# Performance work log

Measured on AMD Instinct MI355X. Metric: run time of the kernel, lower is better.

The kernel has to match this reference:

```python
import jax, jax.numpy as jnp
import numpy as np

ALPHA = 0.2  # LeakyReLU negative slope


def setup_inputs() -> dict:
    key = jax.random.key(0)
    k_x, k_w, k_a = jax.random.split(key, 3)
    B, N, F_in = 4, 2048, 128
    H, nhid = 4, 32  # out_channel=128, nheads=4
    x = jax.random.normal(k_x, (B, N, F_in), dtype=jnp.float32)
    # per-head projection and attention vector, xavier-ish scale
    W = jax.random.normal(k_w, (H, F_in, nhid), dtype=jnp.float32) * (1.414 * np.sqrt(2.0 / (F_in + nhid))) / np.sqrt(3.0) * np.sqrt(3.0)
    a = jax.random.normal(k_a, (H, 2 * nhid), dtype=jnp.float32) * (1.414 * np.sqrt(2.0 / (2 * nhid + 1)))
    return {"x": x, "W": W, "a": a}


def reference(x, W, a):
    # x: [B,N,F_in], W: [H,F_in,d], a: [H,2d]
    H = W.shape[0]
    d = W.shape[2]
    B, N, _ = x.shape
    Wh = jnp.einsum('bni,hij->bhnj', x, W)          # [B,H,N,d]
    a1 = a[:, :d]                                    # [H,d]
    a2 = a[:, d:]                                    # [H,d]
    Wh1 = jnp.einsum('bhnd,hd->bhn', Wh, a1)         # [B,H,N]
    Wh2 = jnp.einsum('bhnd,hd->bhn', Wh, a2)         # [B,H,N]
    e = Wh1[:, :, :, None] + Wh2[:, :, None, :]      # [B,H,N,N]
    e = jnp.where(e > 0, e, ALPHA * e)               # LeakyReLU
    attn = jax.nn.softmax(e, axis=-1)                # softmax over source nodes
    h = jnp.einsum('bhij,bhjd->bhid', attn, Wh)      # [B,H,N,d]
    h = jax.nn.elu(h)
    # concat heads along feature dim: [B,N,H*d]
    out = jnp.transpose(h, (0, 2, 1, 3)).reshape(B, N, H * d)
    return out
```

## Files before the change

kernel.cpp:

```cpp
#include <hip/hip_runtime.h>


#define LOG2E 1.4426950408889634f
constexpr int Nn = 2048, Fin = 128, Dd = 32;

typedef _Float16 half8 __attribute__((ext_vector_type(8)));
typedef _Float16 half4v __attribute__((ext_vector_type(4)));
typedef _Float16 half2v __attribute__((ext_vector_type(2)));
typedef float f32x4 __attribute__((ext_vector_type(4)));

union H8 { half2v h2[4]; half8 h8; };

__global__ __launch_bounds__(256) void k1_wh(
    const float* __restrict__ x, const float* __restrict__ W,
    const float* __restrict__ a, _Float16* __restrict__ whT,
    float* __restrict__ sArr, float* __restrict__ tArr) {
  int blk = blockIdx.x;
  int bh = blk >> 5, tile = blk & 31;
  int b = bh >> 2, h = bh & 3;
  int tid = threadIdx.x, w = tid >> 6, lane = tid & 63;
  int q = lane >> 4, m = lane & 15;
  int rowbase = tile * 64 + w * 16;

  const float* Wq = W + h * Fin * Dd;
  const float* xb = x + (size_t)(b * Nn + rowbase + m) * Fin;

  f32x4 acc[2];
  acc[0] = (f32x4){0.f, 0.f, 0.f, 0.f};
  acc[1] = (f32x4){0.f, 0.f, 0.f, 0.f};

#pragma unroll
  for (int kt = 0; kt < 4; ++kt) {
    float4 x0 = *(const float4*)(xb + kt * 32 + q * 8);
    float4 x1 = *(const float4*)(xb + kt * 32 + q * 8 + 4);
    float xv[8] = {x0.x, x0.y, x0.z, x0.w, x1.x, x1.y, x1.z, x1.w};
    half8 Ah, Al;
#pragma unroll
    for (int j = 0; j < 8; ++j) {
      _Float16 hi = (_Float16)xv[j];
      Ah[j] = hi;
      Al[j] = (_Float16)(xv[j] - (float)hi);
    }
#pragma unroll
    for (int nt = 0; nt < 2; ++nt) {
      half8 Bh, Bl;
#pragma unroll
      for (int j = 0; j < 8; ++j) {
        float wv = Wq[(kt * 32 + q * 8 + j) * Dd + nt * 16 + m];
        _Float16 hi = (_Float16)wv;
        Bh[j] = hi;
        Bl[j] = (_Float16)(wv - (float)hi);
      }
      acc[nt] = __builtin_amdgcn_mfma_f32_16x16x32_f16(Ah, Bh, acc[nt], 0, 0, 0);
      acc[nt] = __builtin_amdgcn_mfma_f32_16x16x32_f16(Al, Bh, acc[nt], 0, 0, 0);
      acc[nt] = __builtin_amdgcn_mfma_f32_16x16x32_f16(Ah, Bl, acc[nt], 0, 0, 0);
    }
  }

#pragma unroll
  for (int nt = 0; nt < 2; ++nt) {
    int d = nt * 16 + m;
    half4v h4;
#pragma unroll
    for (int r = 0; r < 4; ++r) h4[r] = (_Float16)acc[nt][r];
    *(half4v*)(whT + (size_t)(bh * Dd + d) * Nn + rowbase + q * 4) = h4;
  }

  const float* ah = a + h * 2 * Dd;
  float a1m0 = ah[m], a1m1 = ah[16 + m];
  float a2m0 = ah[Dd + m], a2m1 = ah[Dd + 16 + m];
#pragma unroll
  for (int r = 0; r < 4; ++r) {
    float ps = acc[0][r] * a1m0 + acc[1][r] * a1m1;
    float pt = acc[0][r] * a2m0 + acc[1][r] * a2m1;
#pragma unroll
    for (int off = 1; off < 16; off <<= 1) {
      ps += __shfl_xor(ps, off);
      pt += __shfl_xor(pt, off);
    }
    if (m == 0) {
      sArr[bh * Nn + rowbase + q * 4 + r] = ps;
      tArr[bh * Nn + rowbase + q * 4 + r] = pt;
    }
  }
}

__global__ __launch_bounds__(256) void k3_attn(
    const _Float16* __restrict__ whT, const float* __restrict__ sArr,
    const float* __restrict__ tArr, float* __restrict__ out) {
  __shared__ float smem[4 * 64 * 33 + 256];
  _Float16* Ef = (_Float16*)smem;
  _Float16* Ff = (_Float16*)(smem + 1024);
  float* red = smem + 2048;

  int blk = blockIdx.x;
  int bh = blk >> 5, tile = blk & 31;
  int b = bh >> 2, h = bh & 3;
  int tid = threadIdx.x, w = tid >> 6, lane = tid & 63;
  int q = lane >> 4, m = lane & 15;

  float tv[8];
  float mx = -1e30f;
#pragma unroll
  for (int k = 0; k < 8; ++k) {
    tv[k] = tArr[bh * Nn + tid + k * 256];
    mx = fmaxf(mx, tv[k]);
  }
  red[tid] = mx;
  __syncthreads();
  for (int ss = 128; ss > 0; ss >>= 1) {
    if (tid < ss) red[tid] = fmaxf(red[tid], red[tid + ss]);
    __syncthreads();
  }
  float T = red[0];
  __syncthreads();
#pragma unroll
  for (int k = 0; k < 8; ++k) {
    float dt = tv[k] - T;
    Ef[tid + k * 256] = (_Float16)__builtin_amdgcn_exp2f(LOG2E * dt);
    Ff[tid + k * 256] = (_Float16)__builtin_amdgcn_exp2f(0.2f * LOG2E * dt);
  }

  half2v aa[4], bb[4];
#pragma unroll
  for (int t = 0; t < 4; ++t) {
    float es = sArr[bh * Nn + tile * 64 + t * 16 + m] + T;
    float al = __builtin_amdgcn_exp2f(0.8f * LOG2E * fminf(es, 0.f));
    float be = __builtin_amdgcn_exp2f(-0.8f * LOG2E * fmaxf(es, 0.f));
    _Float16 ah_ = (_Float16)al, bh_ = (_Float16)be;
    aa[t] = (half2v){ah_, ah_};
    bb[t] = (half2v){bh_, bh_};
  }
  __syncthreads();

  f32x4 acc[4][2];
#pragma unroll
  for (int t = 0; t < 4; ++t) {
    acc[t][0] = (f32x4){0.f, 0.f, 0.f, 0.f};
    acc[t][1] = (f32x4){0.f, 0.f, 0.f, 0.f};
  }
  float den[4] = {0.f, 0.f, 0.f, 0.f};
  const half2v ones = (half2v){(_Float16)1.f, (_Float16)1.f};

  const _Float16* wb = whT + (size_t)bh * Dd * Nn;

  for (int s = 0; s < 16; ++s) {
    int jb = w * 512 + s * 32;
    half8 B0 = *(const half8*)(wb + (size_t)m * Nn + jb + q * 8);
    half8 B1 = *(const half8*)(wb + (size_t)(16 + m) * Nn + jb + q * 8);
    H8 E, F;
    E.h8 = *(const half8*)&Ef[jb + q * 8];
    F.h8 = *(const half8*)&Ff[jb + q * 8];

#pragma unroll
    for (int t = 0; t < 4; ++t) {
      H8 P;
#pragma unroll
      for (int kk = 0; kk < 4; ++kk) {
        half2v pe = aa[t] * E.h2[kk];
        half2v pf = bb[t] * F.h2[kk];
        half2v p2 = __builtin_elementwise_max(pe, pf);
        P.h2[kk] = p2;
        den[t] = __builtin_amdgcn_fdot2(p2, ones, den[t], false);
      }
      acc[t][0] = __builtin_amdgcn_mfma_f32_16x16x32_f16(P.h8, B0, acc[t][0], 0, 0, 0);
      acc[t][1] = __builtin_amdgcn_mfma_f32_16x16x32_f16(P.h8, B1, acc[t][1], 0, 0, 0);
    }
  }

#pragma unroll
  for (int t = 0; t < 4; ++t) {
    den[t] += __shfl_xor(den[t], 16);
    den[t] += __shfl_xor(den[t], 32);
  }
  __syncthreads();
  float* redN = smem;
  float* redD = smem + 4 * 64 * 33;
#pragma unroll
  for (int t = 0; t < 4; ++t) {
#pragma unroll
    for (int dh = 0; dh < 2; ++dh)
#pragma unroll
      for (int r = 0; r < 4; ++r)
        redN[(w * 64 + t * 16 + q * 4 + r) * 33 + dh * 16 + m] = acc[t][dh][r];
    if (q == 0) redD[w * 64 + t * 16 + m] = den[t];
  }
  __syncthreads();
  {
    int rl = tid >> 2, dg = (tid & 3) * 8;
    float num[8];
#pragma unroll
    for (int i = 0; i < 8; ++i)
      num[i] = redN[(0 * 64 + rl) * 33 + dg + i] + redN[(1 * 64 + rl) * 33 + dg + i] +
               redN[(2 * 64 + rl) * 33 + dg + i] + redN[(3 * 64 + rl) * 33 + dg + i];
    float dt = redD[rl] + redD[64 + rl] + redD[128 + rl] + redD[192 + rl];
    float rd = 1.0f / dt;
    float* orow = out + (size_t)(b * Nn + tile * 64 + rl) * (4 * Dd) + h * Dd + dg;
#pragma unroll
    for (int i = 0; i < 8; ++i) {
      float hv = num[i] * rd;
      num[i] = hv > 0.f ? hv : (__builtin_amdgcn_exp2f(hv * LOG2E) - 1.0f);
    }
    *(float4*)orow = make_float4(num[0], num[1], num[2], num[3]);
    *((float4*)orow + 1) = make_float4(num[4], num[5], num[6], num[7]);
  }
}

extern "C" void kernel_launch(void* const* d_in, const int* in_sizes, int n_in,
                              void* d_out, int out_size, void* d_ws, size_t ws_size,
                              hipStream_t stream) {
  const float* x = (const float*)d_in[0];
  const float* W = (const float*)d_in[1];
  const float* a = (const float*)d_in[2];
  float* out = (float*)d_out;

  float* wsf = (float*)d_ws;
  float* sArr = wsf;
  float* tArr = sArr + 32768;
  _Float16* whT = (_Float16*)(tArr + 32768);

  k1_wh<<<dim3(512), dim3(256), 0, stream>>>(x, W, a, whT, sArr, tArr);
  k3_attn<<<dim3(512), dim3(256), 0, stream>>>(whT, sArr, tArr, out);
}
```

Before: 77.45 us.

## Stage W splits in LDS, prefetch attention operands, compute softmax denominator via MFMA

In the projection kernel, each block now converts W once into hi/lo fp16 halves stored in padded shared memory, replacing the strided scalar global reads that every wave repeated. In the attention kernel, the softmax denominator moves from per-lane fdot2 accumulation plus cross-lane shuffles to an extra MFMA against a one-hot B column. The next iteration's whT and E/F operands are also prefetched into registers (software pipelining). This cuts VALU work and load latency in the hot loop, at the cost of one more MFMA per tile, more registers, and an LDS barrier in the first kernel.

```diff
diff --git a/kernel.cpp b/kernel.cpp
--- a/kernel.cpp
+++ b/kernel.cpp
@@ -15,6 +15,11 @@
     const float* __restrict__ x, const float* __restrict__ W,
     const float* __restrict__ a, _Float16* __restrict__ whT,
     float* __restrict__ sArr, float* __restrict__ tArr) {
+  constexpr int KLD = 136;
+  __shared__ __align__(16) _Float16 Wlds[2 * 32 * KLD];
+  _Float16* BhL = Wlds;
+  _Float16* BlL = Wlds + 32 * KLD;
+
   int blk = blockIdx.x;
   int bh = blk >> 5, tile = blk & 31;
   int b = bh >> 2, h = bh & 3;
@@ -23,8 +28,25 @@
   int rowbase = tile * 64 + w * 16;
 
   const float* Wq = W + h * Fin * Dd;
+  {
+    int k = tid >> 1, dbase = (tid & 1) * 16;
+    const float* wp = Wq + k * Dd + dbase;
+    float4 w0 = *(const float4*)(wp);
+    float4 w1 = *(const float4*)(wp + 4);
+    float4 w2 = *(const float4*)(wp + 8);
+    float4 w3 = *(const float4*)(wp + 12);
+    float wv[16] = {w0.x, w0.y, w0.z, w0.w, w1.x, w1.y, w1.z, w1.w,
+                    w2.x, w2.y, w2.z, w2.w, w3.x, w3.y, w3.z, w3.w};
+#pragma unroll
+    for (int u = 0; u < 16; ++u) {
+      _Float16 hi = (_Float16)wv[u];
+      BhL[(dbase + u) * KLD + k] = hi;
+      BlL[(dbase + u) * KLD + k] = (_Float16)(wv[u] - (float)hi);
+    }
+  }
+  __syncthreads();
+
   const float* xb = x + (size_t)(b * Nn + rowbase + m) * Fin;
-
   f32x4 acc[2];
   acc[0] = (f32x4){0.f, 0.f, 0.f, 0.f};
   acc[1] = (f32x4){0.f, 0.f, 0.f, 0.f};
@@ -43,14 +65,9 @@
     }
 #pragma unroll
     for (int nt = 0; nt < 2; ++nt) {
-      half8 Bh, Bl;
-#pragma unroll
-      for (int j = 0; j < 8; ++j) {
-        float wv = Wq[(kt * 32 + q * 8 + j) * Dd + nt * 16 + m];
-        _Float16 hi = (_Float16)wv;
-        Bh[j] = hi;
-        Bl[j] = (_Float16)(wv - (float)hi);
-      }
+      int off = (nt * 16 + m) * KLD + kt * 32 + q * 8;
+      half8 Bh = *(const half8*)&BhL[off];
+      half8 Bl = *(const half8*)&BlL[off];
       acc[nt] = __builtin_amdgcn_mfma_f32_16x16x32_f16(Ah, Bh, acc[nt], 0, 0, 0);
       acc[nt] = __builtin_amdgcn_mfma_f32_16x16x32_f16(Al, Bh, acc[nt], 0, 0, 0);
       acc[nt] = __builtin_amdgcn_mfma_f32_16x16x32_f16(Ah, Bl, acc[nt], 0, 0, 0);
@@ -134,23 +151,37 @@
   __syncthreads();
 
   f32x4 acc[4][2];
+  f32x4 accd[4];
 #pragma unroll
   for (int t = 0; t < 4; ++t) {
     acc[t][0] = (f32x4){0.f, 0.f, 0.f, 0.f};
     acc[t][1] = (f32x4){0.f, 0.f, 0.f, 0.f};
-  }
-  float den[4] = {0.f, 0.f, 0.f, 0.f};
-  const half2v ones = (half2v){(_Float16)1.f, (_Float16)1.f};
+    accd[t] = (f32x4){0.f, 0.f, 0.f, 0.f};
+  }
+  half8 bden;
+  {
+    _Float16 v = (_Float16)((m == 0) ? 1.f : 0.f);
+#pragma unroll
+    for (int j = 0; j < 8; ++j) bden[j] = v;
+  }
 
   const _Float16* wb = whT + (size_t)bh * Dd * Nn;
-
+  const int jb0 = w * 512;
+
+  half8 B0 = *(const half8*)(wb + (size_t)m * Nn + jb0 + q * 8);
+  half8 B1 = *(const half8*)(wb + (size_t)(16 + m) * Nn + jb0 + q * 8);
+  H8 E, F;
+  E.h8 = *(const half8*)&Ef[jb0 + q * 8];
+  F.h8 = *(const half8*)&Ff[jb0 + q * 8];
+
+#pragma unroll 2
   for (int s = 0; s < 16; ++s) {
-    int jb = w * 512 + s * 32;
-    half8 B0 = *(const half8*)(wb + (size_t)m * Nn + jb + q * 8);
-    half8 B1 = *(const half8*)(wb + (size_t)(16 + m) * Nn + jb + q * 8);
-    H8 E, F;
-    E.h8 = *(const half8*)&Ef[jb + q * 8];
-    F.h8 = *(const half8*)&Ff[jb + q * 8];
+    int jn = jb0 + ((s + 1) & 15) * 32;
+    half8 nB0 = *(const half8*)(wb + (size_t)m * Nn + jn + q * 8);
+    half8 nB1 = *(const half8*)(wb + (size_t)(16 + m) * Nn + jn + q * 8);
+    H8 nE, nF;
+    nE.h8 = *(const half8*)&Ef[jn + q * 8];
+    nF.h8 = *(const half8*)&Ff[jn + q * 8];
 
 #pragma unroll
     for (int t = 0; t < 4; ++t) {
@@ -159,20 +190,15 @@
       for (int kk = 0; kk < 4; ++kk) {
         half2v pe = aa[t] * E.h2[kk];
         half2v pf = bb[t] * F.h2[kk];
-        half2v p2 = __builtin_elementwise_max(pe, pf);
-        P.h2[kk] = p2;
-        den[t] = __builtin_amdgcn_fdot2(p2, ones, den[t], false);
+        P.h2[kk] = __builtin_elementwise_max(pe, pf);
       }
       acc[t][0] = __builtin_amdgcn_mfma_f32_16x16x32_f16(P.h8, B0, acc[t][0], 0, 0, 0);
       acc[t][1] = __builtin_amdgcn_mfma_f32_16x16x32_f16(P.h8, B1, acc[t][1], 0, 0, 0);
-    }
-  }
-
-#pragma unroll
-  for (int t = 0; t < 4; ++t) {
-    den[t] += __shfl_xor(den[t], 16);
-    den[t] += __shfl_xor(den[t], 32);
-  }
+      accd[t]  = __builtin_amdgcn_mfma_f32_16x16x32_f16(P.h8, bden, accd[t], 0, 0, 0);
+    }
+    B0 = nB0; B1 = nB1; E = nE; F = nF;
+  }
+
   __syncthreads();
   float* redN = smem;
   float* redD = smem + 4 * 64 * 33;
@@ -183,7 +209,11 @@
 #pragma unroll
       for (int r = 0; r < 4; ++r)
         redN[(w * 64 + t * 16 + q * 4 + r) * 33 + dh * 16 + m] = acc[t][dh][r];
-    if (q == 0) redD[w * 64 + t * 16 + m] = den[t];
+    if (m == 0) {
+#pragma unroll
+      for (int r = 0; r < 4; ++r)
+        redD[w * 64 + t * 16 + q * 4 + r] = accd[t][r];
+    }
   }
   __syncthreads();
   {
```

Result: no change. 76.43 us (-1.3%).
